# Kernel tuning notes

Measured on AMD Instinct MI355X. Metric: run time of the kernel, lower is better.

## Reference

```python
import math
import jax, jax.numpy as jnp
import numpy as np

N, C, H, W = 32, 64, 96, 96
SHIFT_H, SHIFT_W = 1, -1  # fixed values of the random roll shifts

def _dwconv(x, w, dilation, pad):
    # depthwise conv, x: (n,c,h,w), w: (c,1,kh,kw)
    return jax.lax.conv_general_dilated(
        x, w, window_strides=(1, 1), padding=((pad, pad), (pad, pad)),
        rhs_dilation=(dilation, dilation),
        dimension_numbers=('NCHW', 'OIHW', 'NCHW'),
        feature_group_count=x.shape[1])

def _unfold_1x7_d2(x):
    # F.unfold(x, (1,7), dilation=(1,2), padding=(0,6)) -> (n,c,7,h,w)
    n, c, h, w = x.shape
    xp = jnp.pad(x, ((0, 0), (0, 0), (0, 0), (6, 6)))
    return jnp.stack([xp[..., 2 * k: 2 * k + w] for k in range(7)], axis=2)

def setup_inputs() -> dict:
    key = jax.random.key(0)
    k0, k1, k2, k3, k4, k5 = jax.random.split(key, 6)
    std = 0.1
    return {
        'x':  jax.random.normal(k0, (N, C, H, W), dtype=jnp.float32),
        'w3': jax.random.normal(k1, (C, 1, 5, 5), dtype=jnp.float32) * std,
        'w4': jax.random.normal(k2, (C, 1, 3, 3), dtype=jnp.float32) * std,
        'p5': jax.random.normal(k3, (1, C, C), dtype=jnp.float32) * std,
        'p6': jax.random.normal(k4, (C, 1), dtype=jnp.float32) * std,
        'p8': jax.random.normal(k5, (C, C * 7), dtype=jnp.float32) * std,
    }

def reference(x, w3, w4, p5, p6, p8):
    n, c, h, w = x.shape
    hw = h * w
    t0 = x
    t1 = jnp.roll(jnp.roll(t0, SHIFT_H, axis=2), SHIFT_W, axis=3)
    # channel attention: (n,c,c)
    t2 = jnp.einsum('nci,ndi->ncd', t0.reshape(n, c, hw), t1.reshape(n, c, hw)) / math.sqrt(hw)
    t3 = _dwconv(t1, w3, dilation=1, pad=2)          # (n,c,h,w)
    t4 = _dwconv(t1, w4, dilation=2, pad=2)          # (n,c,h,w)
    t5 = p5 * t2                                      # (n,c,c)
    t6 = jnp.einsum('nchw,ce->nehw', t4, p6).reshape(n, h, w)
    t7 = _unfold_1x7_d2(t0).reshape(n, c * 7, hw)     # (n, c*7, hw)
    t8 = jnp.einsum('nbc,bd->ndc', t5, p8)            # (n, c*7, c)
    t9 = jnp.einsum('nci,ni->nc', t3.reshape(n, c, hw), t6.reshape(n, hw)) / math.sqrt(hw)
    t10 = jnp.einsum('nkc,nks->ncs', t8, t7) / math.sqrt(c * 7)  # (n,c,hw)
    t11 = t9[:, :, None] + t10
    return t11.reshape(n, c, h, w)
```

## Files before the change

kernel.cpp:

```cpp
#include <hip/hip_runtime.h>

#define NB 32
#define CCH 64
#define HH 96
#define WWID 96
#define HWP (HH*WWID)
#define K7 448

#define OFF_T5 2097152
#define OFF_T8 2228224
#define OFF_T6 3145728
#define OFF_T9 3440640

typedef __attribute__((ext_vector_type(8))) short short8;
typedef __attribute__((ext_vector_type(4))) short shortx4;
typedef __attribute__((ext_vector_type(4))) float floatx4;
typedef float __attribute__((ext_vector_type(4), aligned(4))) float4u;

__device__ __forceinline__ short f2bf(float x) {
    unsigned u = __float_as_uint(x);
    unsigned r = (u + 0x7FFF + ((u >> 16) & 1)) >> 16;
    return (short)r;
}

__device__ __forceinline__ void ld_ab(const float* __restrict__ xa, int base,
                                      float4u* va, float4u* vb, int t) {
#pragma unroll
    for (int i = 0; i < 2; i++) {
        int idx = i * 256 + t;
        int c = idx >> 3, k4 = idx & 7;
        int gi = base + k4 * 4;
        const float* xc = xa + c * HWP;
        va[i] = *(const float4u*)(xc + gi);
        int h = gi / WWID, w = gi - h * WWID;
        int hr = (h == 0) ? (HH - 1) : (h - 1);
        const float* xrow = xc + hr * WWID;
        if (w < 92) {
            vb[i] = *(const float4u*)(xrow + w + 1);
        } else {
            float4u tmp;
            tmp.x = xrow[93]; tmp.y = xrow[94]; tmp.z = xrow[95]; tmp.w = xrow[0];
            vb[i] = tmp;
        }
    }
}

__global__ __launch_bounds__(256) void k_t2(const float* __restrict__ x,
                                            float* __restrict__ t2p) {
    int blk = blockIdx.x;
    int n = blk >> 4, sl = blk & 15;
    int k0 = sl * 576;
    __shared__ short ash[64][40];
    __shared__ short bsh[64][40];
    int t = threadIdx.x;
    int lane = t & 63, wv = t >> 6;
    int q = lane >> 4, r16 = lane & 15;
    const float* xa = x + (size_t)n * CCH * HWP;

    floatx4 acc[4] = {};

    float4u va[2], vb[2];
    ld_ab(xa, k0, va, vb, t);

    for (int kc = 0; kc < 576; kc += 32) {
        __syncthreads();
#pragma unroll
        for (int i = 0; i < 2; i++) {
            int idx = i * 256 + t;
            int c = idx >> 3, k4 = idx & 7;
            shortx4 pa = {f2bf(va[i].x), f2bf(va[i].y), f2bf(va[i].z), f2bf(va[i].w)};
            shortx4 pb = {f2bf(vb[i].x), f2bf(vb[i].y), f2bf(vb[i].z), f2bf(vb[i].w)};
            *(shortx4*)&ash[c][k4 * 4] = pa;
            *(shortx4*)&bsh[c][k4 * 4] = pb;
        }
        __syncthreads();
        if (kc + 32 < 576)
            ld_ab(xa, k0 + kc + 32, va, vb, t);
        short8 bfrag = *(const short8*)&bsh[wv * 16 + r16][q * 8];
#pragma unroll
        for (int mi = 0; mi < 4; mi++) {
            short8 afrag = *(const short8*)&ash[mi * 16 + r16][q * 8];
            acc[mi] = __builtin_amdgcn_mfma_f32_16x16x32_bf16(afrag, bfrag, acc[mi], 0, 0, 0);
        }
    }

    float* o = t2p + (size_t)(n * 16 + sl) * 4096;
#pragma unroll
    for (int mi = 0; mi < 4; mi++) {
        int m = mi * 16 + q * 4;
#pragma unroll
        for (int i = 0; i < 4; i++)
            o[(m + i) * 64 + wv * 16 + r16] = acc[mi][i];
    }
}

__global__ __launch_bounds__(256) void k_t5(const float* __restrict__ t2p,
                                            const float* __restrict__ p5,
                                            float* __restrict__ t5) {
    int idx = blockIdx.x * 256 + threadIdx.x;
    int n = idx >> 12, rc = idx & 4095;
    float s = 0.f;
#pragma unroll
    for (int sl = 0; sl < 16; sl++)
        s += t2p[((size_t)n * 16 + sl) * 4096 + rc];
    t5[idx] = s * p5[rc] * (1.0f / 96.0f);
}

__global__ __launch_bounds__(256) void k_t8(const float* __restrict__ t5,
                                            const float* __restrict__ p8,
                                            short* __restrict__ t8t) {
    int n = blockIdx.y;
    int idx = blockIdx.x * 256 + threadIdx.x;
    int k = idx >> 6, c = idx & 63;
    const float* t5n = t5 + (size_t)n * 4096;
    float s = 0.f;
#pragma unroll 8
    for (int b = 0; b < 64; b++)
        s += t5n[b * 64 + c] * p8[b * K7 + k];
    int c7 = k / 7, kk = k - c7 * 7;
    t8t[((size_t)n * 64 + c) * K7 + kk * 64 + c7] = f2bf(s * 0.04724555912f);
}

__global__ __launch_bounds__(256) void k_t6(const float* __restrict__ x,
                                            const float* __restrict__ w4,
                                            const float* __restrict__ p6,
                                            float* __restrict__ t6) {
    int n = blockIdx.y;
    int pix = blockIdx.x * 256 + threadIdx.x;
    int h = pix / WWID, w = pix - h * WWID;

    int off9[9];
    float m9[9];
#pragma unroll
    for (int i = 0; i < 3; i++) {
        int gh = h + (i - 1) * 2;
        bool vr = (gh >= 0) && (gh < HH);
        int srow = vr ? ((gh + HH - 1) % HH) * WWID : 0;
        float rm = vr ? 1.f : 0.f;
#pragma unroll
        for (int j = 0; j < 3; j++) {
            int gw = w + (j - 1) * 2;
            bool vc = (gw >= 0) && (gw < WWID);
            int scol = vc ? (gw + 1) % WWID : 0;
            off9[i * 3 + j] = srow + scol;
            m9[i * 3 + j] = vc ? rm : 0.f;
        }
    }
    const float* xn = x + (size_t)n * CCH * HWP;
    float acc = 0.f;
    for (int c = 0; c < CCH; c++) {
        const float* xc = xn + c * HWP;
        float pw = p6[c];
        const float* wc = w4 + c * 9;
#pragma unroll
        for (int ij = 0; ij < 9; ij++) {
            float wm = wc[ij] * pw * m9[ij];
            acc = fmaf(wm, xc[off9[ij]], acc);
        }
    }
    t6[(size_t)n * HWP + pix] = acc;
}

__global__ __launch_bounds__(256) void k_t9(const float* __restrict__ x,
                                            const float* __restrict__ w3,
                                            const float* __restrict__ t6,
                                            float* __restrict__ t9) {
    int n = blockIdx.y, c = blockIdx.x;
    __shared__ float xl[100][100];
    __shared__ float red[4];
    int t = threadIdx.x;
    const float* xc = x + ((size_t)n * CCH + c) * HWP;
    const float* t6n = t6 + (size_t)n * HWP;

    for (int idx = t; idx < 784; idx += 256) {
        if (idx < 400) {
            int r = idx / 100, col = idx - r * 100;
            int row = r < 2 ? r : r + 96;
            xl[row][col] = 0.f;
        } else {
            int rem = idx - 400;
            int h2 = rem >> 2, c4 = rem & 3;
            int col = c4 < 2 ? c4 : c4 + 96;
            xl[2 + h2][col] = 0.f;
        }
    }
    for (int idx = t; idx < HWP; idx += 256) {
        int h = idx / WWID, w = idx - h * WWID;
        int sh = (h == 0) ? (HH - 1) : (h - 1);
        int sw = (w == WWID - 1) ? 0 : (w + 1);
        xl[h + 2][w + 2] = xc[sh * WWID + sw];
    }
    float wv[25];
#pragma unroll
    for (int i = 0; i < 25; i++) wv[i] = w3[c * 25 + i];
    __syncthreads();

    float acc = 0.f;
#pragma unroll
    for (int g = 0; g < 9; g++) {
        int idx = g * 256 + t;
        int h = idx / 24, wg = idx - h * 24;
        int w0 = wg * 4;
        float4 tv = *(const float4*)(t6n + h * WWID + w0);
        float conv[4] = {0.f, 0.f, 0.f, 0.f};
#pragma unroll
        for (int kh = 0; kh < 5; kh++) {
            float4 ra = *(const float4*)&xl[h + kh][w0];
            float4 rb = *(const float4*)&xl[h + kh][w0 + 4];
            float r[8] = {ra.x, ra.y, ra.z, ra.w, rb.x, rb.y, rb.z, rb.w};
#pragma unroll
            for (int kw = 0; kw < 5; kw++) {
                float wk = wv[kh * 5 + kw];
                conv[0] = fmaf(wk, r[kw],     conv[0]);
                conv[1] = fmaf(wk, r[kw + 1], conv[1]);
                conv[2] = fmaf(wk, r[kw + 2], conv[2]);
                conv[3] = fmaf(wk, r[kw + 3], conv[3]);
            }
        }
        acc = fmaf(conv[0], tv.x, acc);
        acc = fmaf(conv[1], tv.y, acc);
        acc = fmaf(conv[2], tv.z, acc);
        acc = fmaf(conv[3], tv.w, acc);
    }
#pragma unroll
    for (int off = 32; off > 0; off >>= 1) acc += __shfl_down(acc, off, 64);
    if ((t & 63) == 0) red[t >> 6] = acc;
    __syncthreads();
    if (t == 0)
        t9[n * 64 + c] = (red[0] + red[1] + red[2] + red[3]) * (1.0f / 96.0f);
}

__global__ __launch_bounds__(256) void k_out(const float* __restrict__ x,
                                             const short* __restrict__ t8t,
                                             const float* __restrict__ t9,
                                             float* __restrict__ out) {
    int n = blockIdx.y;
    int h0 = blockIdx.x * 2;
    __shared__ short xsh[2 * 108 * 72];
    int t = threadIdx.x;

    for (int idx = t; idx < 2 * 12 * 72; idx += 256) {
        int r = idx / (12 * 72);
        int rem = idx - r * (12 * 72);
        int iwz = rem / 72, c7 = rem - iwz * 72;
        int iw = iwz < 6 ? iwz : iwz + 96;
        xsh[(r * 108 + iw) * 72 + c7] = 0;
    }
    const float* xn = x + (size_t)n * CCH * HWP;
    for (int idx = t; idx < 2 * CCH * 24; idx += 256) {
        int r = idx / (CCH * 24);
        int rem = idx - r * (CCH * 24);
        int c7 = rem / 24, wb = rem - c7 * 24;
        int w0 = wb * 4;
        float4 v = *(const float4*)(xn + c7 * HWP + (h0 + r) * WWID + w0);
        int base = (r * 108 + w0 + 6) * 72 + c7;
        xsh[base]       = f2bf(v.x);
        xsh[base + 72]  = f2bf(v.y);
        xsh[base + 144] = f2bf(v.z);
        xsh[base + 216] = f2bf(v.w);
    }
    __syncthreads();

    int lane = t & 63, wv = t >> 6;
    int q = lane >> 4, sl = lane & 15;
    int mh = wv & 1;
    int sh2 = wv >> 1;
    floatx4 acc[2][6] = {};
    const short* A = t8t + (size_t)n * 64 * K7;

    for (int kc = 0; kc < K7; kc += 32) {
        int kk = kc >> 6;
        int c7b = (kc & 63) + q * 8;
        short8 a[2], b[6];
#pragma unroll
        for (int mi = 0; mi < 2; mi++)
            a[mi] = *(const short8*)(A + ((mh * 2 + mi) * 16 + sl) * K7 + kc + q * 8);
#pragma unroll
        for (int sj = 0; sj < 6; sj++) {
            int iw = sj * 16 + sl + 2 * kk;
            b[sj] = *(const short8*)&xsh[(sh2 * 108 + iw) * 72 + c7b];
        }
#pragma unroll
        for (int mi = 0; mi < 2; mi++)
#pragma unroll
            for (int sj = 0; sj < 6; sj++)
                acc[mi][sj] = __builtin_amdgcn_mfma_f32_16x16x32_bf16(
                    a[mi], b[sj], acc[mi][sj], 0, 0, 0);
    }

    const float* t9n = t9 + n * 64;
#pragma unroll
    for (int mi = 0; mi < 2; mi++) {
#pragma unroll
        for (int i = 0; i < 4; i++) {
            int c = (mh * 2 + mi) * 16 + q * 4 + i;
            float tv = t9n[c];
            float* orow = out + ((size_t)n * CCH + c) * HWP + (h0 + sh2) * WWID;
#pragma unroll
            for (int sj = 0; sj < 6; sj++)
                orow[sj * 16 + sl] = acc[mi][sj][i] + tv;
        }
    }
}

extern "C" void kernel_launch(void* const* d_in, const int* in_sizes, int n_in,
                              void* d_out, int out_size, void* d_ws, size_t ws_size,
                              hipStream_t stream) {
    const float* x  = (const float*)d_in[0];
    const float* w3 = (const float*)d_in[1];
    const float* w4 = (const float*)d_in[2];
    const float* p5 = (const float*)d_in[3];
    const float* p6 = (const float*)d_in[4];
    const float* p8 = (const float*)d_in[5];
    float* out = (float*)d_out;
    float* ws  = (float*)d_ws;

    float* t2p = ws;
    float* t5  = ws + OFF_T5;
    short* t8t = (short*)(ws + OFF_T8);
    float* t6  = ws + OFF_T6;
    float* t9  = ws + OFF_T9;

    k_t2<<<512, 256, 0, stream>>>(x, t2p);
    k_t5<<<512, 256, 0, stream>>>(t2p, p5, t5);
    k_t8<<<dim3(112, 32), 256, 0, stream>>>(t5, p8, t8t);
    k_t6<<<dim3(36, 32), 256, 0, stream>>>(x, w4, p6, t6);
    k_t9<<<dim3(64, 32), 256, 0, stream>>>(x, w3, t6, t9);
    k_out<<<dim3(48, 32), 256, 0, stream>>>(x, t8t, t9, out);
}
```

Before: 270.8 us.

## Swizzle k_out shared-memory tile and drop padding rows to cut LDS footprint

Replaces the padded 108x72 per-row shared-memory layout of the bf16 input tile with a compact 64-wide XOR-swizzled layout. Out-of-range columns now point at a single zero row instead of stored padding. The global load is reorganised so each thread gathers four channels at one pixel and writes them as a packed 4-short store. This reduces the LDS footprint to allow more resident blocks (launch bounds min 6) and aims to cut bank conflicts on the MFMA B-operand reads. The cost is extra index arithmetic and branching per B load, and the global reads become strided scalar loads rather than float4.

After: 407.3 us. 50.4% more time.

```diff
diff --git a/kernel.cpp b/kernel.cpp
--- a/kernel.cpp
+++ b/kernel.cpp
@@ -230,34 +230,28 @@
         t9[n * 64 + c] = (red[0] + red[1] + red[2] + red[3]) * (1.0f / 96.0f);
 }
 
-__global__ __launch_bounds__(256) void k_out(const float* __restrict__ x,
-                                             const short* __restrict__ t8t,
-                                             const float* __restrict__ t9,
-                                             float* __restrict__ out) {
+__global__ __launch_bounds__(256, 6) void k_out(const float* __restrict__ x,
+                                                const short* __restrict__ t8t,
+                                                const float* __restrict__ t9,
+                                                float* __restrict__ out) {
     int n = blockIdx.y;
     int h0 = blockIdx.x * 2;
-    __shared__ short xsh[2 * 108 * 72];
+    __shared__ short xsh[193 * 64];
     int t = threadIdx.x;
 
-    for (int idx = t; idx < 2 * 12 * 72; idx += 256) {
-        int r = idx / (12 * 72);
-        int rem = idx - r * (12 * 72);
-        int iwz = rem / 72, c7 = rem - iwz * 72;
-        int iw = iwz < 6 ? iwz : iwz + 96;
-        xsh[(r * 108 + iw) * 72 + c7] = 0;
-    }
+    if (t < 32) ((int*)xsh)[192 * 32 + t] = 0;
+
     const float* xn = x + (size_t)n * CCH * HWP;
-    for (int idx = t; idx < 2 * CCH * 24; idx += 256) {
-        int r = idx / (CCH * 24);
-        int rem = idx - r * (CCH * 24);
-        int c7 = rem / 24, wb = rem - c7 * 24;
-        int w0 = wb * 4;
-        float4 v = *(const float4*)(xn + c7 * HWP + (h0 + r) * WWID + w0);
-        int base = (r * 108 + w0 + 6) * 72 + c7;
-        xsh[base]       = f2bf(v.x);
-        xsh[base + 72]  = f2bf(v.y);
-        xsh[base + 144] = f2bf(v.z);
-        xsh[base + 216] = f2bf(v.w);
+#pragma unroll
+    for (int i = 0; i < 12; i++) {
+        int idx = i * 256 + t;
+        int r = idx / 1536;
+        int rem = idx - r * 1536;
+        int c7g = rem / 96, w = rem - c7g * 96;
+        const float* src = xn + (size_t)(c7g * 4) * HWP + (h0 + r) * WWID + w;
+        shortx4 p = {f2bf(src[0]), f2bf(src[HWP]), f2bf(src[2 * HWP]), f2bf(src[3 * HWP])};
+        int R = r * 96 + w;
+        *(shortx4*)&xsh[R * 64 + ((c7g * 4) ^ ((R & 7) << 3))] = p;
     }
     __syncthreads();
 
@@ -265,20 +259,26 @@
     int q = lane >> 4, sl = lane & 15;
     int mh = wv & 1;
     int sh2 = wv >> 1;
+    int rbase = sh2 * 96 - 6;
     floatx4 acc[2][6] = {};
     const short* A = t8t + (size_t)n * 64 * K7;
 
     for (int kc = 0; kc < K7; kc += 32) {
         int kk = kc >> 6;
         int c7b = (kc & 63) + q * 8;
+        int iwb = sl + 2 * kk;
         short8 a[2], b[6];
 #pragma unroll
         for (int mi = 0; mi < 2; mi++)
             a[mi] = *(const short8*)(A + ((mh * 2 + mi) * 16 + sl) * K7 + kc + q * 8);
 #pragma unroll
         for (int sj = 0; sj < 6; sj++) {
-            int iw = sj * 16 + sl + 2 * kk;
-            b[sj] = *(const short8*)&xsh[(sh2 * 108 + iw) * 72 + c7b];
+            int iw = sj * 16 + iwb;
+            int Rv;
+            if (sj == 0)      Rv = (iw >= 6)  ? (rbase + iw) : 192;
+            else if (sj == 5) Rv = (iw < 102) ? (rbase + iw) : 192;
+            else              Rv = rbase + iw;
+            b[sj] = *(const short8*)&xsh[Rv * 64 + (c7b ^ ((Rv & 7) << 3))];
         }
 #pragma unroll
         for (int mi = 0; mi < 2; mi++)
```
